# Kernel optimization log

Hardware: AMD Instinct MI355X
Metric: run time of the kernel (lower is better)

The kernel has to match this reference:

```python
import jax, jax.numpy as jnp
import numpy as np

EMB = 1024
HEADS = 16
FFN = 4096
EPS = 1e-5


def _layernorm(x, g, b):
    mu = jnp.mean(x, axis=-1, keepdims=True)
    var = jnp.mean((x - mu) ** 2, axis=-1, keepdims=True)
    return (x - mu) * jax.lax.rsqrt(var + EPS) * g + b


def setup_inputs() -> dict:
    key = jax.random.key(0)
    ks = jax.random.split(key, 8)
    B, T = 2, 2048
    s_in = 1.0 / np.sqrt(EMB)
    s_ffn = 1.0 / np.sqrt(FFN)
    return {
        "x": jax.random.normal(ks[0], (B, T, EMB), jnp.float32),
        "positions": jnp.arange(B * T, dtype=jnp.int64 if jax.config.jax_enable_x64 else jnp.int32).reshape(B, T),
        "ln1_g": jnp.ones((EMB,), jnp.float32),
        "ln1_b": jnp.zeros((EMB,), jnp.float32),
        "ln2_g": jnp.ones((EMB,), jnp.float32),
        "ln2_b": jnp.zeros((EMB,), jnp.float32),
        "Wq": jax.random.normal(ks[1], (EMB, EMB), jnp.float32) * s_in,
        "bq": jnp.zeros((EMB,), jnp.float32),
        "Wk": jax.random.normal(ks[2], (EMB, EMB), jnp.float32) * s_in,
        "bk": jnp.zeros((EMB,), jnp.float32),
        "Wv": jax.random.normal(ks[3], (EMB, EMB), jnp.float32) * s_in,
        "bv": jnp.zeros((EMB,), jnp.float32),
        "Wo": jax.random.normal(ks[4], (EMB, EMB), jnp.float32) * s_in,
        "bo": jnp.zeros((EMB,), jnp.float32),
        "W1": jax.random.normal(ks[5], (EMB, FFN), jnp.float32) * s_in,
        "b1": jnp.zeros((FFN,), jnp.float32),
        "W2": jax.random.normal(ks[6], (FFN, EMB), jnp.float32) * s_ffn,
        "b2": jnp.zeros((EMB,), jnp.float32),
    }


def reference(x, positions, ln1_g, ln1_b, ln2_g, ln2_b,
              Wq, bq, Wk, bk, Wv, bv, Wo, bo, W1, b1, W2, b2):
    B, T, C = x.shape
    H, D = HEADS, C // HEADS
    # x = ln1(x); then residual branches add onto the normalized x (as in source)
    x = _layernorm(x, ln1_g, ln1_b)
    # --- self attention (rope=None, mask=None, dropout inactive) ---
    q = (x @ Wq + bq).reshape(B, T, H, D).transpose(0, 2, 1, 3)  # [B,H,T,D]
    k = (x @ Wk + bk).reshape(B, T, H, D).transpose(0, 2, 1, 3)
    v = (x @ Wv + bv).reshape(B, T, H, D).transpose(0, 2, 1, 3)
    scale = 1.0 / jnp.sqrt(jnp.asarray(D, x.dtype))
    attn = jnp.einsum("bhtd,bhsd->bhts", q, k) * scale  # [B,H,T,T]
    attn = jax.nn.softmax(attn, axis=-1)
    attn_out = jnp.einsum("bhts,bhsd->bhtd", attn, v)
    attn_out = attn_out.transpose(0, 2, 1, 3).reshape(B, T, C)
    attn_out = attn_out @ Wo + bo
    x = x + attn_out
    # --- FFN with exact (erf) GELU, matching torch nn.GELU default ---
    h = _layernorm(x, ln2_g, ln2_b)
    h = jax.nn.gelu(h @ W1 + b1, approximate=False)
    h = h @ W2 + b2
    return x + h
```

## Files before the change

### kernel.cpp

```cpp
#include <hip/hip_runtime.h>
#include <cstdint>
#include <cstddef>

typedef __bf16 bf16;
typedef __bf16 bf16x8 __attribute__((ext_vector_type(8)));
typedef __bf16 bf16x4 __attribute__((ext_vector_type(4)));
typedef float f32x4 __attribute__((ext_vector_type(4)));
typedef float f32x16 __attribute__((ext_vector_type(16)));

#define TOKENS 4096
#define TSEQ   2048
#define NHEADS 16
#define HDIM   64
#define CDIM   1024

typedef __attribute__((address_space(3))) unsigned int lds_uint;
typedef __attribute__((address_space(1))) const unsigned int g_uint;
__device__ __forceinline__ void glds16(const bf16* g, bf16* l) {
  __builtin_amdgcn_global_load_lds((g_uint*)g, (lds_uint*)l, 16, 0, 0);
}

__device__ __forceinline__ float gelu_f(float v) {
  float g2 = v * (1.5957691216f + 0.0713548163f * v * v);
  return v / (1.0f + __expf(-g2));
}

#define NBUF 17
struct DetectArgs { const void* p[NBUF]; int n[NBUF]; };

__global__ __launch_bounds__(256) void detect_kernel(DetectArgs a, int* __restrict__ flags) {
  __shared__ int s_nz, s_bl;
  if (threadIdx.x == 0) { s_nz = 0; s_bl = 0; }
  __syncthreads();
  int i = blockIdx.x;
  const unsigned int* w = (const unsigned int*)a.p[i];
  int nwords = a.n[i] / 2; if (nwords > 2048) nwords = 2048;
  int nz = 0, bl = 0;
  for (int j = threadIdx.x; j < nwords; j += 256) {
    unsigned int v = w[j];
    if (v != 0u) {
      nz++;
      unsigned int e = (v >> 7) & 0xFFu;
      if (e >= 100u && e <= 140u) bl++;
    }
  }
  atomicAdd(&s_nz, nz);
  atomicAdd(&s_bl, bl);
  __syncthreads();
  if (threadIdx.x == 0) flags[i] = (2 * s_bl >= s_nz) ? 1 : 0;
}

__device__ __forceinline__ float ld_any(const void* p, size_t idx, bool isb) {
  return isb ? (float)((const bf16*)p)[idx] : ((const float*)p)[idx];
}

__device__ __forceinline__ void ln_stats(float s, float s2, int tid, float& mu, float& rstd) {
#pragma unroll
  for (int off = 32; off; off >>= 1) {
    s  += __shfl_down(s, off);
    s2 += __shfl_down(s2, off);
  }
  __shared__ float red[8];
  int w = tid >> 6;
  if ((tid & 63) == 0) { red[w] = s; red[4 + w] = s2; }
  __syncthreads();
  if (tid == 0) {
    red[0] = red[0] + red[1] + red[2] + red[3];
    red[4] = red[4] + red[5] + red[6] + red[7];
  }
  __syncthreads();
  mu = red[0] * (1.0f / CDIM);
  float var = fmaxf(red[4] * (1.0f / CDIM) - mu * mu, 0.f);
  rstd = rsqrtf(var + 1e-5f);
}

__global__ __launch_bounds__(256) void ln_f32(const float* __restrict__ x,
                                              const bf16* __restrict__ g,
                                              const bf16* __restrict__ b,
                                              bf16* __restrict__ y) {
  int row = blockIdx.x, tid = threadIdx.x;
  float v[4]; float s = 0.f, s2 = 0.f;
#pragma unroll
  for (int i = 0; i < 4; i++) {
    float f = x[(size_t)row * CDIM + tid * 4 + i];
    v[i] = f; s += f; s2 += f * f;
  }
  float mu, rstd;
  ln_stats(s, s2, tid, mu, rstd);
  bf16* yr = y + (size_t)row * CDIM;
#pragma unroll
  for (int i = 0; i < 4; i++) {
    int c = tid * 4 + i;
    yr[c] = (bf16)((v[i] - mu) * rstd * (float)g[c] + (float)b[c]);
  }
}

struct MegaArgs {
  const void* w_in[6]; bf16* w_out[6]; int wK[6], wN[6], wflag[6];
  const void* vp[10]; bf16* vd[10]; int vn[10], vfi[10];
  const void* x; const void* graw; const void* braw; bf16* y;
};

__global__ __launch_bounds__(256) void mega_pre(MegaArgs a, const int* __restrict__ flags) {
  int bid = blockIdx.x;
  int tx = threadIdx.x, ty = threadIdx.y;
  int tid = tx + ty * 64;
  if (bid < 3072) {
    __shared__ bf16 tile[64][65];
    int mi, start;
    if (bid < 1024)      { mi = bid >> 8; start = mi << 8; }
    else if (bid < 2048) { mi = 4; start = 1024; }
    else                 { mi = 5; start = 2048; }
    int tb = bid - start;
    int nT = a.wN[mi] >> 6;
    int kb = (tb / nT) * 64, nb = (tb % nT) * 64;
    int K = a.wK[mi], N = a.wN[mi];
    bool isb = flags[a.wflag[mi]] != 0;
    const void* in = a.w_in[mi]; bf16* out = a.w_out[mi];
    for (int i = ty; i < 64; i += 4)
      tile[i][tx] = (bf16)ld_any(in, (size_t)(kb + i) * N + nb + tx, isb);
    __syncthreads();
    for (int i = ty; i < 64; i += 4)
      out[(size_t)(nb + i) * K + kb + tx] = tile[tx][i];
  } else if (bid == 3072) {
    for (int i = 0; i < 10; i++) {
      bool isb = flags[a.vfi[i]] != 0;
      const void* in = a.vp[i]; bf16* out = a.vd[i]; int n = a.vn[i];
      for (int j = tid; j < n; j += 256)
        out[j] = (bf16)ld_any(in, j, isb);
    }
  } else {
    int row = bid - 3073;
    bool isb  = flags[0] != 0;
    bool gisb = flags[1] != 0;
    bool bisb = flags[2] != 0;
    float v[4]; float s = 0.f, s2 = 0.f;
#pragma unroll
    for (int i = 0; i < 4; i++) {
      float f = ld_any(a.x, (size_t)row * CDIM + tid * 4 + i, isb);
      v[i] = f; s += f; s2 += f * f;
    }
    float mu, rstd;
    ln_stats(s, s2, tid, mu, rstd);
    bf16* yr = a.y + (size_t)row * CDIM;
#pragma unroll
    for (int i = 0; i < 4; i++) {
      int c = tid * 4 + i;
      float gv = ld_any(a.graw, c, gisb);
      float bv = ld_any(a.braw, c, bisb);
      yr[c] = (bf16)((v[i] - mu) * rstd * gv + bv);
    }
  }
}

template <int BM, int BN>
__device__ __forceinline__ void gemm_core(const bf16* __restrict__ A,
                                          const bf16* __restrict__ Bt,
                                          int K, int m0, int n0,
                                          bf16* As, bf16* Bs,
                                          f32x4 (&acc)[BM / 32][BN / 32]) {
  constexpr int SI = BM / 32, SJ = BN / 32;
  int t = threadIdx.x;
  int wave = t >> 6, lane = t & 63, quad = lane >> 4, l16 = lane & 15;
  int wm = (wave & 1) * (BM / 2), wn = (wave >> 1) * (BN / 2);
  int srow = t >> 2, sc = t & 3;
  int swz = (srow >> 1) & 3;
  const bf16* ga[BM / 64];
  const bf16* gb[BN / 64];
#pragma unroll
  for (int h = 0; h < BM / 64; h++)
    ga[h] = A + (size_t)(m0 + h * 64 + srow) * K + (sc ^ swz) * 8;
#pragma unroll
  for (int h = 0; h < BN / 64; h++)
    gb[h] = Bt + (size_t)(n0 + h * 64 + srow) * K + (sc ^ swz) * 8;

  for (int k0 = 0; k0 < K; k0 += 64) {
#pragma unroll
    for (int q = 0; q < 2; q++) {
#pragma unroll
      for (int h = 0; h < BM / 64; h++)
        glds16(ga[h] + k0 + q * 32, As + q * (BM * 32) + h * 2048 + srow * 32 + sc * 8);
#pragma unroll
      for (int h = 0; h < BN / 64; h++)
        glds16(gb[h] + k0 + q * 32, Bs + q * (BN * 32) + h * 2048 + srow * 32 + sc * 8);
    }
    __syncthreads();
#pragma unroll
    for (int q = 0; q < 2; q++) {
      bf16x8 af[SI], bfr[SJ];
#pragma unroll
      for (int i = 0; i < SI; i++) {
        int m = wm + i * 16 + l16;
        af[i] = *(const bf16x8*)&As[q * (BM * 32) + m * 32 + ((quad ^ ((m >> 1) & 3)) * 8)];
      }
#pragma unroll
      for (int j = 0; j < SJ; j++) {
        int n = wn + j * 16 + l16;
        bfr[j] = *(const bf16x8*)&Bs[q * (BN * 32) + n * 32 + ((quad ^ ((n >> 1) & 3)) * 8)];
      }
#pragma unroll
      for (int i = 0; i < SI; i++)
#pragma unroll
        for (int j = 0; j < SJ; j++)
          acc[i][j] = __builtin_amdgcn_mfma_f32_16x16x32_bf16(af[i], bfr[j], acc[i][j], 0, 0, 0);
    }
    __syncthreads();
  }
}

#define EPI_NONE 0
#define EPI_RES  1
#define EPI_GELU 2

template <int BM, int BN, int EPI, typename OutT, typename ResT>
__global__ __launch_bounds__(256) void gemm128(const bf16* __restrict__ A,
                                               const bf16* __restrict__ Bt,
                                               const bf16* __restrict__ bias,
                                               const ResT* __restrict__ res,
                                               OutT* __restrict__ C,
                                               int N, int K) {
  __shared__ alignas(16) bf16 As[2 * BM * 32];
  __shared__ alignas(16) bf16 Bs[2 * BN * 32];
  int m0 = blockIdx.y * BM, n0 = blockIdx.x * BN;
  f32x4 acc[BM / 32][BN / 32] = {};
  gemm_core<BM, BN>(A, Bt, K, m0, n0, As, Bs, acc);

  int t = threadIdx.x, wave = t >> 6, lane = t & 63, quad = lane >> 4, l16 = lane & 15;
  int wm = (wave & 1) * (BM / 2), wn = (wave >> 1) * (BN / 2);
#pragma unroll
  for (int i = 0; i < BM / 32; i++)
#pragma unroll
    for (int j = 0; j < BN / 32; j++) {
      int n = n0 + wn + j * 16 + l16;
      float bv = (float)bias[n];
#pragma unroll
      for (int r = 0; r < 4; r++) {
        int m = m0 + wm + i * 16 + quad * 4 + r;
        float v = acc[i][j][r] + bv;
        if (EPI == EPI_GELU)      v = gelu_f(v);
        else if (EPI == EPI_RES)  v += (float)res[(size_t)m * N + n];
        C[(size_t)m * N + n] = (OutT)v;
      }
    }
}

__device__ __forceinline__ void gemm256_core(const bf16* __restrict__ A,
                                             const bf16* __restrict__ Bt,
                                             int K, int lda, int ldb, int m0, int n0,
                                             bf16* sm, f32x4 (&acc)[8][4]) {
  const int NT = K >> 6;
  const int t = threadIdx.x;
  const int lane = t & 63, quad = lane >> 4, l16 = lane & 15;
  const int wave = t >> 6;
  const int wm = (wave & 1) * 128, wn = (wave >> 1) * 64;
  const int srow = t >> 2, sc = t & 3;
  const int swz = (srow >> 1) & 3;
  const int rA = (srow & 63) + ((srow >> 6) << 7);
  const bf16* gA = A + (size_t)(m0 + rA) * lda + ((sc ^ swz) << 3);
  const bf16* gB = Bt + (size_t)(n0 + srow) * ldb + ((sc ^ swz) << 3);
  const int ldsA = rA * 32 + sc * 8;
  const int ldsB = srow * 32 + sc * 8;

  auto stA = [&](int tile, int u) {
    if (tile >= NT) return;
    const bf16* g = gA + (size_t)(u << 6) * lda + (tile << 6);
    bf16* l = sm + ((tile & 1) << 15) + ldsA + (u << 11);
    glds16(g, l);
    glds16(g + 32, l + 8192);
  };
  auto stB = [&](int tile, int h) {
    if (tile >= NT) return;
    const bf16* g = gB + (size_t)(h << 7) * ldb + (tile << 6);
    bf16* l = sm + ((tile & 1) << 15) + 16384 + ldsB + (h << 12);
    glds16(g, l);
    glds16(g + 32, l + 8192);
  };

  stB(0, 0); stB(0, 1); stA(0, 0); stA(0, 1);
  stB(1, 0); stB(1, 1); stA(1, 0);
  asm volatile("s_waitcnt vmcnt(6)" ::: "memory");
  __builtin_amdgcn_s_barrier();
  asm volatile("" ::: "memory");

  bf16x8 bfr[2][4];

#define LDB256(buf)                                                        \
  _Pragma("unroll") for (int q = 0; q < 2; q++)                            \
  _Pragma("unroll") for (int j = 0; j < 4; j++) {                          \
    int nl = wn + j * 16 + l16;                                            \
    bfr[q][j] = *(const bf16x8*)&sm[((buf) << 15) + 16384 + q * 8192 +     \
                                    nl * 32 + ((quad ^ ((nl >> 1) & 3)) << 3)]; \
  }

#define PHASE256(buf, P, STAGE, EXTRAWAIT)                                 \
  {                                                                        \
    bf16x8 af[2][2];                                                       \
    _Pragma("unroll") for (int q = 0; q < 2; q++)                          \
    _Pragma("unroll") for (int i2 = 0; i2 < 2; i2++) {                     \
      int ml = wm + (P) * 32 + i2 * 16 + l16;                              \
      af[q][i2] = *(const bf16x8*)&sm[((buf) << 15) + q * 8192 + ml * 32 + \
                                      ((quad ^ ((ml >> 1) & 3)) << 3)];    \
    }                                                                      \
    if ((P) == 0) { LDB256(buf); }                                         \
    STAGE;                                                                 \
    asm volatile("" ::: "memory");                                         \
    __builtin_amdgcn_s_barrier();                                          \
    asm volatile("s_waitcnt lgkmcnt(0)" ::: "memory");                     \
    __builtin_amdgcn_s_setprio(1);                                         \
    _Pragma("unroll") for (int q = 0; q < 2; q++)                          \
    _Pragma("unroll") for (int i2 = 0; i2 < 2; i2++)                       \
    _Pragma("unroll") for (int j = 0; j < 4; j++)                          \
      acc[(P) * 2 + i2][j] = __builtin_amdgcn_mfma_f32_16x16x32_bf16(      \
          af[q][i2], bfr[q][j], acc[(P) * 2 + i2][j], 0, 0, 0);            \
    __builtin_amdgcn_s_setprio(0);                                         \
    asm volatile("" ::: "memory");                                         \
    EXTRAWAIT;                                                             \
    __builtin_amdgcn_s_barrier();                                          \
    asm volatile("" ::: "memory");                                         \
  }

  for (int t0 = 0; t0 < NT; t0 += 2) {
    const int t1 = t0 + 1;
    PHASE256(0, 0, stA(t1, 1), (void)0);
    PHASE256(0, 1, stB(t0 + 2, 0), (void)0);
    PHASE256(0, 2, stB(t0 + 2, 1), (void)0);
    PHASE256(0, 3, stA(t0 + 2, 0),
             asm volatile("s_waitcnt vmcnt(6)" ::: "memory"));
    PHASE256(1, 0, stA(t0 + 2, 1), (void)0);
    PHASE256(1, 1, stB(t1 + 2, 0), (void)0);
    PHASE256(1, 2, stB(t1 + 2, 1), (void)0);
    PHASE256(1, 3, stA(t1 + 2, 0),
             asm volatile("s_waitcnt vmcnt(6)" ::: "memory"));
  }
#undef PHASE256
#undef LDB256
}

__device__ __forceinline__ void xcd_swizzle(int& bx, int& by) {
  int gx = gridDim.x;
  int nwg = gx * gridDim.y;
  int bid = blockIdx.x + blockIdx.y * gx;
  int wg = (bid & 7) * (nwg >> 3) + (bid >> 3);
  bx = wg % gx; by = wg / gx;
}

__global__ __launch_bounds__(512, 2) void gemm256_gelu(const bf16* __restrict__ A,
                                                       const bf16* __restrict__ Bt,
                                                       const bf16* __restrict__ bias,
                                                       bf16* __restrict__ C,
                                                       int N, int K) {
  __shared__ alignas(16) bf16 sm[65536];
  int bx, by; xcd_swizzle(bx, by);
  int m0 = by * 256, n0 = bx * 256;
  f32x4 acc[8][4] = {};
  gemm256_core(A, Bt, K, K, K, m0, n0, sm, acc);

  int t = threadIdx.x, wave = t >> 6, lane = t & 63, quad = lane >> 4, l16 = lane & 15;
  int wm = (wave & 1) * 128, wn = (wave >> 1) * 64;
#pragma unroll
  for (int i = 0; i < 8; i++)
#pragma unroll
    for (int j = 0; j < 4; j++) {
      int n = n0 + wn + j * 16 + l16;
      float bv = (float)bias[n];
#pragma unroll
      for (int r = 0; r < 4; r++) {
        int m = m0 + wm + i * 16 + quad * 4 + r;
        C[(size_t)m * N + n] = (bf16)gelu_f(acc[i][j][r] + bv);
      }
    }
}

__global__ __launch_bounds__(512, 2) void gemm256_part(const bf16* __restrict__ A,
                                                       const bf16* __restrict__ Bt,
                                                       bf16* __restrict__ P0, bf16* __restrict__ P1,
                                                       bf16* __restrict__ P2, bf16* __restrict__ P3,
                                                       int lda) {
  __shared__ alignas(16) bf16 sm[65536];
  int m0 = blockIdx.y * 256, n0 = blockIdx.x * 256, kz = blockIdx.z;
  const bf16* Ak = A + (size_t)kz * 1024;
  const bf16* Bk = Bt + (size_t)kz * 1024;
  f32x4 acc[8][4] = {};
  gemm256_core(Ak, Bk, 1024, lda, lda, m0, n0, sm, acc);

  bf16* P = (kz == 0) ? P0 : (kz == 1) ? P1 : (kz == 2) ? P2 : P3;
  int t = threadIdx.x, wave = t >> 6, lane = t & 63, quad = lane >> 4, l16 = lane & 15;
  int wm = (wave & 1) * 128, wn = (wave >> 1) * 64;
#pragma unroll
  for (int i = 0; i < 8; i++)
#pragma unroll
    for (int j = 0; j < 4; j++) {
      int n = n0 + wn + j * 16 + l16;
#pragma unroll
      for (int r = 0; r < 4; r++) {
        int m = m0 + wm + i * 16 + quad * 4 + r;
        P[(size_t)m * 1024 + n] = (bf16)acc[i][j][r];
      }
    }
}

__global__ __launch_bounds__(256) void w2_reduce(const bf16* __restrict__ P0, const bf16* __restrict__ P1,
                                                 const bf16* __restrict__ P2, const bf16* __restrict__ P3,
                                                 const float* __restrict__ res, const bf16* __restrict__ bias,
                                                 float* __restrict__ out) {
  int c = threadIdx.x * 4;
  size_t base = (size_t)blockIdx.x * 1024 + c;
  bf16x4 a0 = *(const bf16x4*)&P0[base];
  bf16x4 a1 = *(const bf16x4*)&P1[base];
  bf16x4 a2 = *(const bf16x4*)&P2[base];
  bf16x4 a3 = *(const bf16x4*)&P3[base];
  f32x4 rv = *(const f32x4*)&res[base];
  f32x4 o;
#pragma unroll
  for (int i = 0; i < 4; i++)
    o[i] = ((float)a0[i] + (float)a1[i]) + ((float)a2[i] + (float)a3[i]) + rv[i] + (float)bias[c + i];
  *(f32x4*)&out[base] = o;
}

__global__ __launch_bounds__(512, 2) void gemm256_qkv(const bf16* __restrict__ A,
                                                      const bf16* __restrict__ Bt,
                                                      const bf16* __restrict__ bias,
                                                      bf16* __restrict__ QK,
                                                      bf16* __restrict__ Vt) {
  __shared__ alignas(16) bf16 sm[65536];
  int bx, by; xcd_swizzle(bx, by);
  int m0 = by * 256, n0 = bx * 256;
  f32x4 acc[8][4] = {};
  gemm256_core(A, Bt, 1024, 1024, 1024, m0, n0, sm, acc);

  int t = threadIdx.x, wave = t >> 6, lane = t & 63, quad = lane >> 4, l16 = lane & 15;
  int wm = (wave & 1) * 128, wn = (wave >> 1) * 64;
#pragma unroll
  for (int i = 0; i < 8; i++)
#pragma unroll
    for (int j = 0; j < 4; j++) {
      int n = n0 + wn + j * 16 + l16;
      float bv = (float)bias[n];
      int mb = m0 + wm + i * 16 + quad * 4;
      if (n < 1024) {
#pragma unroll
        for (int r = 0; r < 4; r++)
          QK[(size_t)(mb + r) * 2048 + n] = (bf16)((acc[i][j][r] + bv) * 0.18033688011112042f);
      } else if (n < 2048) {
#pragma unroll
        for (int r = 0; r < 4; r++)
          QK[(size_t)(mb + r) * 2048 + n] = (bf16)(acc[i][j][r] + bv);
      } else {
        int qt = (mb >> 2) & 3;
        int qt2 = ((qt & 1) << 1) | (qt >> 1);
        int mb2 = (mb & ~15) | (qt2 << 2);
        bf16x4 pk;
#pragma unroll
        for (int r = 0; r < 4; r++) pk[r] = (bf16)(acc[i][j][r] + bv);
        *(bf16x4*)&Vt[(size_t)(n - 2048) * TOKENS + mb2] = pk;
      }
    }
}

__global__ __launch_bounds__(256, 3) void attn_kernel(const bf16* __restrict__ QK,
                                                      const bf16* __restrict__ Vt,
                                                      bf16* __restrict__ O) {
  __shared__ alignas(16) bf16 KV[3][8192];
  int bid = blockIdx.x;
  int xcd = bid & 7, slot = bid >> 3;
  int g = xcd + 8 * (slot >> 4);
  int q0 = (slot & 15) * 128;
  int h = g & 15, b = g >> 4;
  int t = threadIdx.x, wave = t >> 6, lane = t & 63;
  int l31 = lane & 31, l5 = lane >> 5, l7 = lane & 7;

  const bf16* Qg = QK;
  const bf16* Kg = QK + 1024;
  const size_t bT = (size_t)b * TSEQ;
  const int h64 = h * 64;

  int sr = lane >> 3;
  int sch = l7 ^ sr;
  auto stage = [&](int tile, int buf) {
    size_t krow = bT + tile * 64 + wave * 8 + sr;
    bf16* kd = &KV[buf][wave * 512 + lane * 8];
    glds16(&Kg[krow * 2048 + h64 + sch * 8], kd);
    glds16(&Kg[(krow + 32) * 2048 + h64 + sch * 8], kd + 2048);
    size_t vrow = (size_t)(h64 + wave * 8 + sr) * TOKENS + bT + tile * 64 + sch * 8;
    glds16(&Vt[vrow], kd + 4096);
    glds16(&Vt[vrow + (size_t)32 * TOKENS], kd + 6144);
  };

  bf16x8 qf[4];
  {
    size_t qrow = bT + q0 + wave * 32 + l31;
    const bf16* qp = &Qg[qrow * 2048 + h64 + l5 * 8];
#pragma unroll
    for (int ds = 0; ds < 4; ds++) qf[ds] = *(const bf16x8*)(qp + ds * 16);
  }

  int off[4];
#pragma unroll
  for (int w = 0; w < 4; w++) off[w] = l31 * 64 + (((w * 2 + l5) ^ l7) * 8);

  f32x16 accO0 = {}, accO1 = {}, accL = {};
  const bf16 one = (bf16)1.0f;
  const bf16x8 onesv = {one, one, one, one, one, one, one, one};

  stage(0, 0);
  stage(1, 1);
  asm volatile("s_waitcnt vmcnt(4)" ::: "memory");
  __builtin_amdgcn_s_barrier();
  asm volatile("" ::: "memory");

  int cur = 0, sb = 2;
  for (int it = 0; it < TSEQ / 64; it++) {
    if (it + 2 < TSEQ / 64) stage(it + 2, sb);
    const bf16* KB = &KV[cur][0];

    f32x16 st0 = {}, st1 = {};
    __builtin_amdgcn_s_setprio(1);
#pragma unroll
    for (int ds = 0; ds < 4; ds++) {
      bf16x8 k0 = *(const bf16x8*)&KB[off[ds]];
      bf16x8 k1 = *(const bf16x8*)&KB[off[ds] + 2048];
      st0 = __builtin_amdgcn_mfma_f32_32x32x16_bf16(k0, qf[ds], st0, 0, 0, 0);
      st1 = __builtin_amdgcn_mfma_f32_32x32x16_bf16(k1, qf[ds], st1, 0, 0, 0);
    }
    __builtin_amdgcn_s_setprio(0);

    bf16x8 pa[4];
#pragma unroll
    for (int j = 0; j < 8; j++) {
      pa[0][j] = (bf16)exp2f(fminf(st0[j], 86.f));
      pa[1][j] = (bf16)exp2f(fminf(st0[8 + j], 86.f));
      pa[2][j] = (bf16)exp2f(fminf(st1[j], 86.f));
      pa[3][j] = (bf16)exp2f(fminf(st1[8 + j], 86.f));
    }

    __builtin_amdgcn_s_setprio(1);
#pragma unroll
    for (int w = 0; w < 4; w++) {
      bf16x8 v0 = *(const bf16x8*)&KB[off[w] + 4096];
      bf16x8 v1 = *(const bf16x8*)&KB[off[w] + 6144];
      accO0 = __builtin_amdgcn_mfma_f32_32x32x16_bf16(pa[w], v0, accO0, 0, 0, 0);
      accO1 = __builtin_amdgcn_mfma_f32_32x32x16_bf16(pa[w], v1, accO1, 0, 0, 0);
      accL  = __builtin_amdgcn_mfma_f32_32x32x16_bf16(pa[w], onesv, accL, 0, 0, 0);
    }
    __builtin_amdgcn_s_setprio(0);

    if (it + 2 < TSEQ / 64)
      asm volatile("s_waitcnt vmcnt(4)" ::: "memory");
    else
      asm volatile("s_waitcnt vmcnt(0)" ::: "memory");
    __builtin_amdgcn_s_barrier();
    asm volatile("" ::: "memory");

    cur = (cur == 2) ? 0 : cur + 1;
    sb  = (sb == 2) ? 0 : sb + 1;
  }

#pragma unroll
  for (int r = 0; r < 16; r++) {
    int q = (r & 3) + 8 * (r >> 2) + 4 * l5;
    float rl = 1.0f / fmaxf(accL[r], 1e-30f);
    size_t orow = (bT + q0 + wave * 32 + q) * CDIM + h64;
    O[orow + l31]      = (bf16)(accO0[r] * rl);
    O[orow + 32 + l31] = (bf16)(accO1[r] * rl);
  }
}

extern "C" void kernel_launch(void* const* d_in, const int* in_sizes, int n_in,
                              void* d_out, int out_size, void* d_ws, size_t ws_size,
                              hipStream_t stream) {
  char* ws = (char*)d_ws;
  const size_t MB = 1024 * 1024;
  const size_t KB = 1024;

  int* flags = (int*)ws;
  bf16* vec_c = (bf16*)(ws + 4 * KB);
  bf16* ln1g_c = vec_c + 0 * 8192;
  bf16* ln1b_c = vec_c + 1 * 8192;
  bf16* ln2g_c = vec_c + 2 * 8192;
  bf16* ln2b_c = vec_c + 3 * 8192;
  bf16* bqkv_c = vec_c + 4 * 8192;
  bf16* bo_c   = vec_c + 6 * 8192;
  bf16* b1_c   = vec_c + 7 * 8192;
  bf16* b2_c   = vec_c + 8 * 8192;

  bf16*  WqkvT  = (bf16*)(ws + 1 * MB);
  bf16*  WoT    = (bf16*)(ws + 7 * MB);
  bf16*  W1T    = (bf16*)(ws + 9 * MB);
  bf16*  W2T    = (bf16*)(ws + 17 * MB);
  bf16*  xn     = (bf16*)(ws + 25 * MB);
  bf16*  QKbuf  = (bf16*)(ws + 33 * MB);
  bf16*  Vtbuf  = (bf16*)(ws + 49 * MB);
  bf16*  ab     = (bf16*)(ws + 57 * MB);
  float* xmid32 = (float*)(ws + 65 * MB);
  bf16*  h2     = (bf16*)(ws + 81 * MB);
  bf16*  f1     = (bf16*)(ws + 33 * MB);
  bf16*  pk0    = (bf16*)(ws + 25 * MB);
  bf16*  pk1    = (bf16*)(ws + 81 * MB);
  bf16*  pk2    = (bf16*)(ws + 1 * MB);
  bf16*  pk3    = (bf16*)(ws + 9 * MB);

  const int din_idx[NBUF] = {0, 2, 3, 4, 5, 6, 7, 8, 9, 10, 11, 12, 13, 14, 15, 16, 17};
  DetectArgs da;
  for (int i = 0; i < NBUF; i++) { da.p[i] = d_in[din_idx[i]]; da.n[i] = in_sizes[din_idx[i]]; }
  detect_kernel<<<NBUF, 256, 0, stream>>>(da, flags);

  MegaArgs ma;
  {
    const void* wi[6] = {d_in[6], d_in[8], d_in[10], d_in[12], d_in[14], d_in[16]};
    bf16* wo[6] = {WqkvT, WqkvT + 1024 * 1024, WqkvT + 2 * 1024 * 1024, WoT, W1T, W2T};
    const int wK[6] = {1024, 1024, 1024, 1024, 1024, 4096};
    const int wN[6] = {1024, 1024, 1024, 1024, 4096, 1024};
    const int wf[6] = {5, 7, 9, 11, 13, 15};
    for (int i = 0; i < 6; i++) {
      ma.w_in[i] = wi[i]; ma.w_out[i] = wo[i];
      ma.wK[i] = wK[i]; ma.wN[i] = wN[i]; ma.wflag[i] = wf[i];
    }
    const int vf[10] = {1, 2, 3, 4, 6, 8, 10, 12, 14, 16};
    bf16* vd[10] = {ln1g_c, ln1b_c, ln2g_c, ln2b_c,
                    bqkv_c, bqkv_c + 1024, bqkv_c + 2048, bo_c, b1_c, b2_c};
    for (int i = 0; i < 10; i++) {
      int di = din_idx[vf[i]];
      ma.vp[i] = d_in[di]; ma.vd[i] = vd[i]; ma.vn[i] = in_sizes[di]; ma.vfi[i] = vf[i];
    }
    ma.x = d_in[0]; ma.graw = d_in[2]; ma.braw = d_in[3]; ma.y = xn;
  }
  mega_pre<<<3072 + 1 + TOKENS, dim3(64, 4), 0, stream>>>(ma, flags);

  gemm256_qkv<<<dim3(12, 16), 512, 0, stream>>>(xn, WqkvT, bqkv_c, QKbuf, Vtbuf);

  attn_kernel<<<512, 256, 0, stream>>>(QKbuf, Vtbuf, ab);

  gemm128<64, 128, EPI_RES, float, bf16><<<dim3(8, 64), 256, 0, stream>>>(
      ab, WoT, bo_c, xn, xmid32, 1024, 1024);

  ln_f32<<<TOKENS, 256, 0, stream>>>(xmid32, ln2g_c, ln2b_c, h2);

  gemm256_gelu<<<dim3(16, 16), 512, 0, stream>>>(h2, W1T, b1_c, f1, 4096, 1024);

  gemm256_part<<<dim3(4, 16, 4), 512, 0, stream>>>(f1, W2T, pk0, pk1, pk2, pk3, 4096);
  w2_reduce<<<TOKENS, 256, 0, stream>>>(pk0, pk1, pk2, pk3, xmid32, b2_c, (float*)d_out);
}
```

Measured before the change: 368.1 us.

## Split attention over two KV halves with combine kernel; vectorize LN and weight transpose

```diff
diff --git a/kernel.cpp b/kernel.cpp
--- a/kernel.cpp
+++ b/kernel.cpp
@@ -79,20 +79,18 @@
                                               const bf16* __restrict__ b,
                                               bf16* __restrict__ y) {
   int row = blockIdx.x, tid = threadIdx.x;
-  float v[4]; float s = 0.f, s2 = 0.f;
-#pragma unroll
-  for (int i = 0; i < 4; i++) {
-    float f = x[(size_t)row * CDIM + tid * 4 + i];
-    v[i] = f; s += f; s2 += f * f;
-  }
+  f32x4 v = *(const f32x4*)&x[(size_t)row * CDIM + tid * 4];
+  float s = v[0] + v[1] + v[2] + v[3];
+  float s2 = v[0] * v[0] + v[1] * v[1] + v[2] * v[2] + v[3] * v[3];
   float mu, rstd;
   ln_stats(s, s2, tid, mu, rstd);
-  bf16* yr = y + (size_t)row * CDIM;
-#pragma unroll
-  for (int i = 0; i < 4; i++) {
-    int c = tid * 4 + i;
-    yr[c] = (bf16)((v[i] - mu) * rstd * (float)g[c] + (float)b[c]);
-  }
+  bf16x4 gv = *(const bf16x4*)&g[tid * 4];
+  bf16x4 bv = *(const bf16x4*)&b[tid * 4];
+  bf16x4 o;
+#pragma unroll
+  for (int i = 0; i < 4; i++)
+    o[i] = (bf16)((v[i] - mu) * rstd * (float)gv[i] + (float)bv[i]);
+  *(bf16x4*)&y[(size_t)row * CDIM + tid * 4] = o;
 }
 
 struct MegaArgs {
@@ -106,7 +104,7 @@
   int tx = threadIdx.x, ty = threadIdx.y;
   int tid = tx + ty * 64;
   if (bid < 3072) {
-    __shared__ bf16 tile[64][65];
+    __shared__ bf16 tile[64][68];
     int mi, start;
     if (bid < 1024)      { mi = bid >> 8; start = mi << 8; }
     else if (bid < 2048) { mi = 4; start = 1024; }
@@ -117,11 +115,30 @@
     int K = a.wK[mi], N = a.wN[mi];
     bool isb = flags[a.wflag[mi]] != 0;
     const void* in = a.w_in[mi]; bf16* out = a.w_out[mi];
-    for (int i = ty; i < 64; i += 4)
-      tile[i][tx] = (bf16)ld_any(in, (size_t)(kb + i) * N + nb + tx, isb);
+    int r0 = tid >> 4, c4 = (tid & 15) * 4;
+#pragma unroll
+    for (int p = 0; p < 4; p++) {
+      int r = r0 + p * 16;
+      size_t gi = (size_t)(kb + r) * N + nb + c4;
+      bf16x4 pk;
+      if (isb) {
+        pk = *(const bf16x4*)&((const bf16*)in)[gi];
+      } else {
+        f32x4 f = *(const f32x4*)&((const float*)in)[gi];
+#pragma unroll
+        for (int j = 0; j < 4; j++) pk[j] = (bf16)f[j];
+      }
+      *(bf16x4*)&tile[r][c4] = pk;
+    }
     __syncthreads();
-    for (int i = ty; i < 64; i += 4)
-      out[(size_t)(nb + i) * K + kb + tx] = tile[tx][i];
+#pragma unroll
+    for (int p = 0; p < 4; p++) {
+      int nr = r0 + p * 16;
+      bf16x4 o;
+#pragma unroll
+      for (int j = 0; j < 4; j++) o[j] = tile[c4 + j][nr];
+      *(bf16x4*)&out[(size_t)(nb + nr) * K + kb + c4] = o;
+    }
   } else if (bid == 3072) {
     for (int i = 0; i < 10; i++) {
       bool isb = flags[a.vfi[i]] != 0;
@@ -135,21 +152,27 @@
     bool gisb = flags[1] != 0;
     bool bisb = flags[2] != 0;
     float v[4]; float s = 0.f, s2 = 0.f;
-#pragma unroll
-    for (int i = 0; i < 4; i++) {
-      float f = ld_any(a.x, (size_t)row * CDIM + tid * 4 + i, isb);
-      v[i] = f; s += f; s2 += f * f;
+    size_t xi = (size_t)row * CDIM + tid * 4;
+    if (isb) {
+      bf16x4 x4 = *(const bf16x4*)&((const bf16*)a.x)[xi];
+#pragma unroll
+      for (int i = 0; i < 4; i++) { v[i] = (float)x4[i]; s += v[i]; s2 += v[i] * v[i]; }
+    } else {
+      f32x4 x4 = *(const f32x4*)&((const float*)a.x)[xi];
+#pragma unroll
+      for (int i = 0; i < 4; i++) { v[i] = x4[i]; s += v[i]; s2 += v[i] * v[i]; }
     }
     float mu, rstd;
     ln_stats(s, s2, tid, mu, rstd);
-    bf16* yr = a.y + (size_t)row * CDIM;
+    bf16x4 o;
 #pragma unroll
     for (int i = 0; i < 4; i++) {
       int c = tid * 4 + i;
       float gv = ld_any(a.graw, c, gisb);
       float bv = ld_any(a.braw, c, bisb);
-      yr[c] = (bf16)((v[i] - mu) * rstd * gv + bv);
-    }
+      o[i] = (bf16)((v[i] - mu) * rstd * gv + bv);
+    }
+    *(bf16x4*)&a.y[(size_t)row * CDIM + tid * 4] = o;
   }
 }
 
@@ -457,14 +480,19 @@
     }
 }
 
-__global__ __launch_bounds__(256, 3) void attn_kernel(const bf16* __restrict__ QK,
+__global__ __launch_bounds__(256, 4) void attn_kernel(const bf16* __restrict__ QK,
                                                       const bf16* __restrict__ Vt,
-                                                      bf16* __restrict__ O) {
-  __shared__ alignas(16) bf16 KV[3][8192];
+                                                      bf16* __restrict__ Oa,
+                                                      bf16* __restrict__ Ob,
+                                                      float* __restrict__ La,
+                                                      float* __restrict__ Lb) {
+  __shared__ alignas(16) bf16 KV[4][8192];
   int bid = blockIdx.x;
   int xcd = bid & 7, slot = bid >> 3;
-  int g = xcd + 8 * (slot >> 4);
-  int q0 = (slot & 15) * 128;
+  int g = xcd + 8 * (slot >> 5);
+  int sub = slot & 31;
+  int q0 = (sub & 15) * 128;
+  int half = sub >> 4;
   int h = g & 15, b = g >> 4;
   int t = threadIdx.x, wave = t >> 6, lane = t & 63;
   int l31 = lane & 31, l5 = lane >> 5, l7 = lane & 7;
@@ -473,15 +501,18 @@
   const bf16* Kg = QK + 1024;
   const size_t bT = (size_t)b * TSEQ;
   const int h64 = h * 64;
+  const int kv0 = half * 1024;
+  bf16* Op = half ? Ob : Oa;
+  float* Lp = half ? Lb : La;
 
   int sr = lane >> 3;
   int sch = l7 ^ sr;
   auto stage = [&](int tile, int buf) {
-    size_t krow = bT + tile * 64 + wave * 8 + sr;
+    size_t krow = bT + kv0 + tile * 64 + wave * 8 + sr;
     bf16* kd = &KV[buf][wave * 512 + lane * 8];
     glds16(&Kg[krow * 2048 + h64 + sch * 8], kd);
     glds16(&Kg[(krow + 32) * 2048 + h64 + sch * 8], kd + 2048);
-    size_t vrow = (size_t)(h64 + wave * 8 + sr) * TOKENS + bT + tile * 64 + sch * 8;
+    size_t vrow = (size_t)(h64 + wave * 8 + sr) * TOKENS + bT + kv0 + tile * 64 + sch * 8;
     glds16(&Vt[vrow], kd + 4096);
     glds16(&Vt[vrow + (size_t)32 * TOKENS], kd + 6144);
   };
@@ -508,9 +539,9 @@
   __builtin_amdgcn_s_barrier();
   asm volatile("" ::: "memory");
 
-  int cur = 0, sb = 2;
-  for (int it = 0; it < TSEQ / 64; it++) {
-    if (it + 2 < TSEQ / 64) stage(it + 2, sb);
+  for (int it = 0; it < 16; it++) {
+    int cur = it & 3;
+    if (it + 2 < 16) stage(it + 2, (it + 2) & 3);
     const bf16* KB = &KV[cur][0];
 
     f32x16 st0 = {}, st1 = {};
@@ -544,25 +575,39 @@
     }
     __builtin_amdgcn_s_setprio(0);
 
-    if (it + 2 < TSEQ / 64)
+    if (it + 2 < 16)
       asm volatile("s_waitcnt vmcnt(4)" ::: "memory");
     else
       asm volatile("s_waitcnt vmcnt(0)" ::: "memory");
     __builtin_amdgcn_s_barrier();
     asm volatile("" ::: "memory");
-
-    cur = (cur == 2) ? 0 : cur + 1;
-    sb  = (sb == 2) ? 0 : sb + 1;
   }
 
 #pragma unroll
   for (int r = 0; r < 16; r++) {
     int q = (r & 3) + 8 * (r >> 2) + 4 * l5;
-    float rl = 1.0f / fmaxf(accL[r], 1e-30f);
-    size_t orow = (bT + q0 + wave * 32 + q) * CDIM + h64;
-    O[orow + l31]      = (bf16)(accO0[r] * rl);
-    O[orow + 32 + l31] = (bf16)(accO1[r] * rl);
-  }
+    size_t row = bT + q0 + wave * 32 + q;
+    Op[row * CDIM + h64 + l31]      = (bf16)accO0[r];
+    Op[row * CDIM + h64 + 32 + l31] = (bf16)accO1[r];
+    if (l31 == 0) Lp[row * 16 + h] = accL[r];
+  }
+}
+
+__global__ __launch_bounds__(256) void attn_combine(bf16* __restrict__ Oa,
+                                                    const bf16* __restrict__ Ob,
+                                                    const float* __restrict__ La,
+                                                    const float* __restrict__ Lb) {
+  int row = blockIdx.x, c = threadIdx.x * 4;
+  size_t base = (size_t)row * CDIM + c;
+  int h = c >> 6;
+  float rl = 1.0f / fmaxf(La[row * 16 + h] + Lb[row * 16 + h], 1e-30f);
+  bf16x4 a = *(const bf16x4*)&Oa[base];
+  bf16x4 b4 = *(const bf16x4*)&Ob[base];
+  bf16x4 o;
+#pragma unroll
+  for (int i = 0; i < 4; i++)
+    o[i] = (bf16)(((float)a[i] + (float)b4[i]) * rl);
+  *(bf16x4*)&Oa[base] = o;
 }
 
 extern "C" void kernel_launch(void* const* d_in, const int* in_sizes, int n_in,
@@ -591,6 +636,9 @@
   bf16*  QKbuf  = (bf16*)(ws + 33 * MB);
   bf16*  Vtbuf  = (bf16*)(ws + 49 * MB);
   bf16*  ab     = (bf16*)(ws + 57 * MB);
+  bf16*  obuf   = (bf16*)(ws + 81 * MB);
+  float* labuf  = (float*)(ws + 65 * MB);
+  float* lbbuf  = (float*)(ws + 65 * MB + 512 * KB);
   float* xmid32 = (float*)(ws + 65 * MB);
   bf16*  h2     = (bf16*)(ws + 81 * MB);
   bf16*  f1     = (bf16*)(ws + 33 * MB);
@@ -628,7 +676,8 @@
 
   gemm256_qkv<<<dim3(12, 16), 512, 0, stream>>>(xn, WqkvT, bqkv_c, QKbuf, Vtbuf);
 
-  attn_kernel<<<512, 256, 0, stream>>>(QKbuf, Vtbuf, ab);
+  attn_kernel<<<1024, 256, 0, stream>>>(QKbuf, Vtbuf, ab, obuf, labuf, lbbuf);
+  attn_combine<<<TOKENS, 256, 0, stream>>>(ab, obuf, labuf, lbbuf);
 
   gemm128<64, 128, EPI_RES, float, bf16><<<dim3(8, 64), 256, 0, stream>>>(
       ab, WoT, bo_c, xn, xmid32, 1024, 1024);
```

New measurement: 394.2 us. +7.1%, slower.
